# Kernel optimization log

Hardware: AMD Instinct MI355X
Metric: run time of the kernel (lower is better)

Reference implementation:

```python
import jax, jax.numpy as jnp
import numpy as np

B, C, D, H, W = 2, 32, 96, 96, 96
RED = 16
INV_SQRT2 = 0.7071067811865476  # 1/sqrt(2), Haar analysis filter coefficient
BN_EPS = 1e-5


def _haar1(x, axis):
    # pywt 'haar' DWT on even-length signals: a[i]=(x[2i]+x[2i+1])/sqrt2, d[i]=(x[2i]-x[2i+1])/sqrt2
    e = jax.lax.slice_in_dim(x, 0, None, stride=2, axis=axis)
    o = jax.lax.slice_in_dim(x, 1, None, stride=2, axis=axis)
    return (e + o) * INV_SQRT2, (e - o) * INV_SQRT2


def haar_dwt3d(x):
    # x: (B, C, D, H, W). Separable 3D Haar DWT; key letters follow pywt dwtn
    # axis order (D, H, W): 'aad' = approx along D, approx along H, detail along W.
    aD, dD = _haar1(x, 2)
    aa, ad = _haar1(aD, 3)
    da, dd = _haar1(dD, 3)
    aaa, aad = _haar1(aa, 4)
    ada, add = _haar1(ad, 4)
    daa, dad = _haar1(da, 4)
    dda, ddd = _haar1(dd, 4)
    # per-channel grouping of 7 detail bands, then flatten to (B, 7C, D/2, H/2, W/2)
    high = jnp.stack([aad, ada, add, daa, dad, dda, ddd], axis=2)
    b, c = x.shape[0], x.shape[1]
    high = high.reshape(b, c * 7, *aaa.shape[2:])
    return aaa, high


def chan_attn(x, w1, w2):
    # AdaptiveAvgPool3d(1) -> FC(no bias) -> ReLU -> FC(no bias) -> Sigmoid -> scale
    y = x.mean(axis=(2, 3, 4))                     # (B, Ch)
    y = jax.nn.sigmoid(jnp.maximum(y @ w1.T, 0.0) @ w2.T)
    return x * y[:, :, None, None, None]


def setup_inputs() -> dict:
    key = jax.random.key(0)
    ks = jax.random.split(key, 7)
    x = jax.random.normal(ks[0], (B, C, D, H, W), dtype=jnp.float32)
    w1_low = jax.random.normal(ks[1], (C // RED, C), dtype=jnp.float32) * 0.1
    w2_low = jax.random.normal(ks[2], (C, C // RED), dtype=jnp.float32) * 0.1
    w1_high = jax.random.normal(ks[3], (7 * C // RED, 7 * C), dtype=jnp.float32) * 0.05
    w2_high = jax.random.normal(ks[4], (7 * C, 7 * C // RED), dtype=jnp.float32) * 0.05
    w_fuse = jax.random.normal(ks[5], (C, 8 * C), dtype=jnp.float32) * 0.05  # 1x1x1 conv kernel
    b_fuse = jnp.zeros((C,), dtype=jnp.float32)
    gamma = jnp.ones((C,), dtype=jnp.float32)
    beta = jnp.zeros((C,), dtype=jnp.float32)
    return dict(x=x, w1_low=w1_low, w2_low=w2_low, w1_high=w1_high, w2_high=w2_high,
                w_fuse=w_fuse, b_fuse=b_fuse, gamma=gamma, beta=beta)


def reference(x, w1_low, w2_low, w1_high, w2_high, w_fuse, b_fuse, gamma, beta):
    low, high = haar_dwt3d(x)                                  # (B,C,48,48,48), (B,7C,48,48,48)
    low = chan_attn(low, w1_low, w2_low)
    high = chan_attn(high, w1_high, w2_high)
    z = jnp.concatenate([low, high], axis=1)                   # (B, 8C, 48,48,48)
    z = jnp.einsum('bcdhw,oc->bodhw', z, w_fuse) + b_fuse[None, :, None, None, None]
    # BatchNorm3d (training-mode batch statistics, as fresh torch module defaults)
    mu = z.mean(axis=(0, 2, 3, 4), keepdims=True)
    var = z.var(axis=(0, 2, 3, 4), keepdims=True)
    z = (z - mu) * jax.lax.rsqrt(var + BN_EPS)
    z = z * gamma[None, :, None, None, None] + beta[None, :, None, None, None]
    return jnp.maximum(z, 0.0)
```

## Files before the change

### kernel.cpp

```cpp
#include <hip/hip_runtime.h>
#include <math.h>

#define HS 0.35355339059327373f
#define NSPAT 110592
#define NBN   221184

__global__ __launch_bounds__(256) void k1_parity(const float* __restrict__ x,
                                                 float* __restrict__ S) {
    int blk = blockIdx.x;
    int d   = blk % 96;
    int bc  = blk / 96;
    const float4* x4 = (const float4*)x + (long)blk * 2304;
    int tid = threadIdx.x;
    float aE0 = 0.f, aO0 = 0.f, aE1 = 0.f, aO1 = 0.f;
#pragma unroll
    for (int i = 0; i < 9; ++i) {
        int f = tid + i * 256;
        float4 v = x4[f];
        int h = f / 24;
        float e = v.x + v.z, o = v.y + v.w;
        if (h & 1) { aE1 += e; aO1 += o; }
        else       { aE0 += e; aO0 += o; }
    }
#pragma unroll
    for (int m = 32; m; m >>= 1) {
        aE0 += __shfl_xor(aE0, m, 64); aO0 += __shfl_xor(aO0, m, 64);
        aE1 += __shfl_xor(aE1, m, 64); aO1 += __shfl_xor(aO1, m, 64);
    }
    __shared__ float red[4][4];
    int lane = tid & 63, wave = tid >> 6;
    if (lane == 0) { red[wave][0] = aE0; red[wave][1] = aO0;
                     red[wave][2] = aE1; red[wave][3] = aO1; }
    __syncthreads();
    if (tid < 4) {
        float v = red[0][tid] + red[1][tid] + red[2][tid] + red[3][tid];
        int q = tid >> 1, r = tid & 1, p = d & 1;
        atomicAdd(&S[bc * 8 + p * 4 + q * 2 + r], v);
    }
}

__global__ __launch_bounds__(256) void k2_attn(
        const float* __restrict__ S,
        const float* __restrict__ w1l, const float* __restrict__ w2l,
        const float* __restrict__ w1h, const float* __restrict__ w2h,
        const float* __restrict__ wf, float* __restrict__ A) {
    int b = blockIdx.x, tid = threadIdx.x;
    __shared__ float mlow[32], mhigh[224], h1l[2], h1h[14], ylow[32], yhigh[224];
    const float* Sb = S + b * 256;
    const float MS = HS / (float)NSPAT;
    if (tid < 32) {
        float s = 0.f;
        for (int j = 0; j < 8; ++j) s += Sb[tid * 8 + j];
        mlow[tid] = s * MS;
    }
    if (tid < 224) {
        int c = tid / 7, k = tid % 7, dm = k + 1;
        float s = 0.f;
        for (int j = 0; j < 8; ++j) {
            float sg = (__popc(j & dm) & 1) ? -1.f : 1.f;
            s += sg * Sb[c * 8 + j];
        }
        mhigh[tid] = s * MS;
    }
    __syncthreads();
    if (tid < 2) {
        float s = 0.f;
        for (int c = 0; c < 32; ++c) s += w1l[tid * 32 + c] * mlow[c];
        h1l[tid] = fmaxf(s, 0.f);
    } else if (tid < 16) {
        int j = tid - 2;
        float s = 0.f;
        for (int c = 0; c < 224; ++c) s += w1h[j * 224 + c] * mhigh[c];
        h1h[j] = fmaxf(s, 0.f);
    }
    __syncthreads();
    if (tid < 32) {
        float s = w2l[tid * 2] * h1l[0] + w2l[tid * 2 + 1] * h1l[1];
        ylow[tid] = 1.f / (1.f + expf(-s));
    } else if (tid < 256) {
        int i = tid - 32;
        float s = 0.f;
        for (int j = 0; j < 14; ++j) s += w2h[i * 14 + j] * h1h[j];
        yhigh[i] = 1.f / (1.f + expf(-s));
    }
    __syncthreads();
    for (int idx = tid; idx < 8192; idx += 256) {
        int o = idx >> 8, c = (idx >> 3) & 31, pqr = idx & 7;
        float a = wf[o * 256 + c] * ylow[c];
#pragma unroll
        for (int k = 0; k < 7; ++k) {
            float sg = (__popc(pqr & (k + 1)) & 1) ? -1.f : 1.f;
            a += sg * wf[o * 256 + 32 + c * 7 + k] * yhigh[c * 7 + k];
        }
        A[b * 8192 + idx] = a * HS;
    }
}

__global__ __launch_bounds__(192) void k3_main(const float* __restrict__ x,
                                               const float* __restrict__ A,
                                               float* __restrict__ z,
                                               float* __restrict__ bnSum,
                                               float* __restrict__ bnSq) {
    __shared__ float ldsA[8192];
    __shared__ float red[3][64];
    int blk = blockIdx.x;
    int b   = blk / 288;
    int rem = blk % 288;
    int od  = rem / 6;
    int ohg = rem % 6;
    int tid = threadIdx.x;
    for (int i = tid; i < 8192; i += 192) ldsA[i] = A[b * 8192 + i];
    __syncthreads();

    int row = tid / 24;
    int t   = tid % 24;
    int oh  = ohg * 8 + row;

    float acc0[32], acc1[32];
#pragma unroll
    for (int o = 0; o < 32; ++o) { acc0[o] = 0.f; acc1[o] = 0.f; }

    const float4* x4 = (const float4*)x;
    int base = (((b * 32) * 96 + 2 * od) * 96 + 2 * oh) * 24 + t;
    for (int c = 0; c < 32; ++c) {
        int i4 = base + c * 221184;
        float4 v00 = x4[i4];
        float4 v01 = x4[i4 + 24];
        float4 v10 = x4[i4 + 2304];
        float4 v11 = x4[i4 + 2304 + 24];
        const float* Ac = &ldsA[c * 8];
#pragma unroll
        for (int o = 0; o < 32; ++o) {
            const float4* Ao = (const float4*)(Ac + o * 256);
            float4 a0 = Ao[0];
            float4 a1 = Ao[1];
            acc0[o] += a0.x * v00.x + a0.y * v00.y + a0.z * v01.x + a0.w * v01.y
                     + a1.x * v10.x + a1.y * v10.y + a1.z * v11.x + a1.w * v11.y;
            acc1[o] += a0.x * v00.z + a0.y * v00.w + a0.z * v01.z + a0.w * v01.w
                     + a1.x * v10.z + a1.y * v10.w + a1.z * v11.z + a1.w * v11.w;
        }
    }

    float2* z2 = (float2*)z;
#pragma unroll
    for (int o = 0; o < 32; ++o) {
        int zi = (((b * 32 + o) * 48 + od) * 48 + oh) * 24 + t;
        z2[zi] = make_float2(acc0[o], acc1[o]);
    }

    int lane = tid & 63, wave = tid >> 6;
#pragma unroll
    for (int o = 0; o < 32; ++o) {
        float sv = acc0[o] + acc1[o];
        float qv = acc0[o] * acc0[o] + acc1[o] * acc1[o];
#pragma unroll
        for (int m = 32; m; m >>= 1) {
            sv += __shfl_xor(sv, m, 64);
            qv += __shfl_xor(qv, m, 64);
        }
        if (lane == 0) { red[wave][o] = sv; red[wave][32 + o] = qv; }
    }
    __syncthreads();
    if (tid < 64) {
        float v = red[0][tid] + red[1][tid] + red[2][tid];
        if (tid < 32) atomicAdd(&bnSum[tid], v);
        else          atomicAdd(&bnSq[tid - 32], v);
    }
}

__global__ void k4_fin(const float* __restrict__ bnSum, const float* __restrict__ bnSq,
                       const float* __restrict__ gamma, const float* __restrict__ beta,
                       float* __restrict__ scale, float* __restrict__ shift) {
    int o = threadIdx.x;
    if (o < 32) {
        const float invN = 1.f / (float)NBN;
        float mean = bnSum[o] * invN;
        float var  = bnSq[o] * invN - mean * mean;
        float inv  = rsqrtf(var + 1e-5f);
        float sc   = gamma[o] * inv;
        scale[o] = sc;
        shift[o] = beta[o] - mean * sc;
    }
}

__global__ __launch_bounds__(256) void k5_norm(float* __restrict__ z,
                                               const float* __restrict__ scale,
                                               const float* __restrict__ shift) {
    int i = blockIdx.x * 256 + threadIdx.x;
    float4* z4 = (float4*)z;
    float4 v = z4[i];
    int o = (i / 27648) & 31;
    float sc = scale[o], sh = shift[o];
    v.x = fmaxf(v.x * sc + sh, 0.f);
    v.y = fmaxf(v.y * sc + sh, 0.f);
    v.z = fmaxf(v.z * sc + sh, 0.f);
    v.w = fmaxf(v.w * sc + sh, 0.f);
    z4[i] = v;
}

extern "C" void kernel_launch(void* const* d_in, const int* in_sizes, int n_in,
                              void* d_out, int out_size, void* d_ws, size_t ws_size,
                              hipStream_t stream) {
    const float* x    = (const float*)d_in[0];
    const float* w1l  = (const float*)d_in[1];
    const float* w2l  = (const float*)d_in[2];
    const float* w1h  = (const float*)d_in[3];
    const float* w2h  = (const float*)d_in[4];
    const float* wf   = (const float*)d_in[5];
    const float* gamma = (const float*)d_in[7];
    const float* beta  = (const float*)d_in[8];
    float* out = (float*)d_out;

    float* ws    = (float*)d_ws;
    float* S     = ws;
    float* bnSum = ws + 512;
    float* bnSq  = ws + 544;
    float* scale = ws + 576;
    float* shift = ws + 608;
    float* A     = ws + 1024;

    hipMemsetAsync(d_ws, 0, 640 * sizeof(float), stream);
    k1_parity<<<6144, 256, 0, stream>>>(x, S);
    k2_attn<<<2, 256, 0, stream>>>(S, w1l, w2l, w1h, w2h, wf, A);
    k3_main<<<576, 192, 0, stream>>>(x, A, out, bnSum, bnSq);
    k4_fin<<<1, 64, 0, stream>>>(bnSum, bnSq, gamma, beta, scale, shift);
    k5_norm<<<6912, 256, 0, stream>>>(out, scale, shift);
}
```

Before: 526.0 us.

## Split output channels across k3 blocks and fold BN finalize into norm kernel

The main fused DWT+conv kernel now gives each block half of the 32 output channels, doubling the grid to 1152 blocks and halving per-thread accumulators and LDS use. The intent is to raise occupancy and improve latency hiding on a grid that was small relative to the CU count. The cost is that each x element is loaded twice, once per channel half. Separately, the tiny BN finalize kernel is removed and each normalization block recomputes scale and shift in shared memory, saving a launch.

New measurement: 468.8 us. -10.9%, faster.

```diff
diff --git a/kernel.cpp b/kernel.cpp
--- a/kernel.cpp
+++ b/kernel.cpp
@@ -101,24 +101,27 @@
                                                float* __restrict__ z,
                                                float* __restrict__ bnSum,
                                                float* __restrict__ bnSq) {
-    __shared__ float ldsA[8192];
-    __shared__ float red[3][64];
+    __shared__ float ldsA[4096];
+    __shared__ float red[3][32];
     int blk = blockIdx.x;
-    int b   = blk / 288;
-    int rem = blk % 288;
-    int od  = rem / 6;
-    int ohg = rem % 6;
+    int og  = blk & 1;
+    int tmp = blk >> 1;
+    int ohg = tmp % 6;
+    tmp /= 6;
+    int od  = tmp % 48;
+    int b   = tmp / 48;
     int tid = threadIdx.x;
-    for (int i = tid; i < 8192; i += 192) ldsA[i] = A[b * 8192 + i];
+    const float* Ab = A + b * 8192 + og * 4096;
+    for (int i = tid; i < 4096; i += 192) ldsA[i] = Ab[i];
     __syncthreads();
 
     int row = tid / 24;
     int t   = tid % 24;
     int oh  = ohg * 8 + row;
 
-    float acc0[32], acc1[32];
-#pragma unroll
-    for (int o = 0; o < 32; ++o) { acc0[o] = 0.f; acc1[o] = 0.f; }
+    float acc0[16], acc1[16];
+#pragma unroll
+    for (int o = 0; o < 16; ++o) { acc0[o] = 0.f; acc1[o] = 0.f; }
 
     const float4* x4 = (const float4*)x;
     int base = (((b * 32) * 96 + 2 * od) * 96 + 2 * oh) * 24 + t;
@@ -130,7 +133,7 @@
         float4 v11 = x4[i4 + 2304 + 24];
         const float* Ac = &ldsA[c * 8];
 #pragma unroll
-        for (int o = 0; o < 32; ++o) {
+        for (int o = 0; o < 16; ++o) {
             const float4* Ao = (const float4*)(Ac + o * 256);
             float4 a0 = Ao[0];
             float4 a1 = Ao[1];
@@ -143,14 +146,14 @@
 
     float2* z2 = (float2*)z;
 #pragma unroll
-    for (int o = 0; o < 32; ++o) {
-        int zi = (((b * 32 + o) * 48 + od) * 48 + oh) * 24 + t;
+    for (int o = 0; o < 16; ++o) {
+        int zi = (((b * 32 + og * 16 + o) * 48 + od) * 48 + oh) * 24 + t;
         z2[zi] = make_float2(acc0[o], acc1[o]);
     }
 
     int lane = tid & 63, wave = tid >> 6;
 #pragma unroll
-    for (int o = 0; o < 32; ++o) {
+    for (int o = 0; o < 16; ++o) {
         float sv = acc0[o] + acc1[o];
         float qv = acc0[o] * acc0[o] + acc1[o] * acc1[o];
 #pragma unroll
@@ -158,39 +161,38 @@
             sv += __shfl_xor(sv, m, 64);
             qv += __shfl_xor(qv, m, 64);
         }
-        if (lane == 0) { red[wave][o] = sv; red[wave][32 + o] = qv; }
-    }
-    __syncthreads();
-    if (tid < 64) {
+        if (lane == 0) { red[wave][o] = sv; red[wave][16 + o] = qv; }
+    }
+    __syncthreads();
+    if (tid < 32) {
         float v = red[0][tid] + red[1][tid] + red[2][tid];
-        if (tid < 32) atomicAdd(&bnSum[tid], v);
-        else          atomicAdd(&bnSq[tid - 32], v);
-    }
-}
-
-__global__ void k4_fin(const float* __restrict__ bnSum, const float* __restrict__ bnSq,
-                       const float* __restrict__ gamma, const float* __restrict__ beta,
-                       float* __restrict__ scale, float* __restrict__ shift) {
-    int o = threadIdx.x;
-    if (o < 32) {
+        if (tid < 16) atomicAdd(&bnSum[og * 16 + tid], v);
+        else          atomicAdd(&bnSq[og * 16 + tid - 16], v);
+    }
+}
+
+__global__ __launch_bounds__(256) void k5_norm(float* __restrict__ z,
+                                               const float* __restrict__ bnSum,
+                                               const float* __restrict__ bnSq,
+                                               const float* __restrict__ gamma,
+                                               const float* __restrict__ beta) {
+    __shared__ float s_sc[32], s_sh[32];
+    int tid = threadIdx.x;
+    if (tid < 32) {
         const float invN = 1.f / (float)NBN;
-        float mean = bnSum[o] * invN;
-        float var  = bnSq[o] * invN - mean * mean;
+        float mean = bnSum[tid] * invN;
+        float var  = bnSq[tid] * invN - mean * mean;
         float inv  = rsqrtf(var + 1e-5f);
-        float sc   = gamma[o] * inv;
-        scale[o] = sc;
-        shift[o] = beta[o] - mean * sc;
-    }
-}
-
-__global__ __launch_bounds__(256) void k5_norm(float* __restrict__ z,
-                                               const float* __restrict__ scale,
-                                               const float* __restrict__ shift) {
-    int i = blockIdx.x * 256 + threadIdx.x;
+        float sc   = gamma[tid] * inv;
+        s_sc[tid] = sc;
+        s_sh[tid] = beta[tid] - mean * sc;
+    }
+    int i = blockIdx.x * 256 + tid;
     float4* z4 = (float4*)z;
     float4 v = z4[i];
+    __syncthreads();
     int o = (i / 27648) & 31;
-    float sc = scale[o], sh = shift[o];
+    float sc = s_sc[o], sh = s_sh[o];
     v.x = fmaxf(v.x * sc + sh, 0.f);
     v.y = fmaxf(v.y * sc + sh, 0.f);
     v.z = fmaxf(v.z * sc + sh, 0.f);
@@ -215,14 +217,11 @@
     float* S     = ws;
     float* bnSum = ws + 512;
     float* bnSq  = ws + 544;
-    float* scale = ws + 576;
-    float* shift = ws + 608;
     float* A     = ws + 1024;
 
-    hipMemsetAsync(d_ws, 0, 640 * sizeof(float), stream);
+    hipMemsetAsync(d_ws, 0, 576 * sizeof(float), stream);
     k1_parity<<<6144, 256, 0, stream>>>(x, S);
     k2_attn<<<2, 256, 0, stream>>>(S, w1l, w2l, w1h, w2h, wf, A);
-    k3_main<<<576, 192, 0, stream>>>(x, A, out, bnSum, bnSq);
-    k4_fin<<<1, 64, 0, stream>>>(bnSum, bnSq, gamma, beta, scale, shift);
-    k5_norm<<<6912, 256, 0, stream>>>(out, scale, shift);
-}
+    k3_main<<<1152, 192, 0, stream>>>(x, A, out, bnSum, bnSq);
+    k5_norm<<<6912, 256, 0, stream>>>(out, bnSum, bnSq, gamma, beta);
+}
```
